# Kernel tuning notes

Hardware: AMD Instinct MI355X
Metric: run time of the kernel (lower is better)

The kernel has to match this reference:

```python
import jax, jax.numpy as jnp
import numpy as np

N = 256
IL_MMI = 0.02      # insertion loss MMI
IMB = 0.01         # imbalance MMI
IL_CR = 0.02       # insertion loss Crossing
CT = 0.01          # cross talk Crossing


def _mmi_matrix():
    # 2x2 MMI: sqrt(1-IL)*[[t, i r],[i r, t]] with t=sqrt((1+imb)/2), r=sqrt((1-imb)/2)
    a = np.sqrt(1.0 - IL_MMI)
    t = np.sqrt((1.0 + IMB) / 2.0)
    r = np.sqrt((1.0 - IMB) / 2.0)
    mmi2 = a * np.array([[t, 1j * r], [1j * r, t]], dtype=np.complex64)
    # block-diagonal over even pairs (0,1),(2,3),...
    return jnp.asarray(np.kron(np.eye(N // 2, dtype=np.complex64), mmi2))


def _crossing_matrix():
    # pairs start at odd index 1; rows 0 and N-1 pass through with amplitude sqrt(1-IL)*sqrt(1-CT)
    a = np.sqrt(1.0 - IL_CR)
    thru = a * np.sqrt(1.0 - CT)
    cr2 = a * np.array([[np.sqrt(CT), 1j * np.sqrt(1.0 - CT)],
                        [1j * np.sqrt(1.0 - CT), np.sqrt(CT)]], dtype=np.complex64)
    M = np.zeros((N, N), dtype=np.complex64)
    M[0, 0] = thru
    for i in range(1, N - 1, 2):
        M[i:i + 2, i:i + 2] = cr2
    if N % 2 == 0:
        M[-1, -1] = thru
    return jnp.asarray(M)


def setup_inputs() -> dict:
    key = jax.random.key(0)
    thetas = jax.random.uniform(key, (N // 2 + 2, N), dtype=jnp.float32) * (2.0 * np.pi)
    return {"thetas": thetas}


def reference(thetas):
    MMI = _mmi_matrix()
    CR = _crossing_matrix()
    phases = jnp.exp(1j * thetas)  # [N//2+2, N] complex64; diag phase-shift layers

    # arch = ht[0] @ I  (diagonal left-multiply == row scaling)
    arch0 = jnp.diag(phases[0])

    def body(arch, ph):
        # one mesh stage with trailing crossing (iterations i = 0 .. N//2-2)
        arch = MMI @ arch
        arch = ph[:, None] * arch      # ht[i+1] @ arch
        arch = MMI @ arch
        arch = CR @ arch
        return arch, None

    arch, _ = jax.lax.scan(body, arch0, phases[1:N // 2])

    # last loop iteration (i = N//2-1): no crossing
    arch = MMI @ arch
    arch = phases[N // 2][:, None] * arch
    arch = MMI @ arch
    # final phase layer ht[N//2+1]
    arch = phases[N // 2 + 1][:, None] * arch
    return arch
```

## Files before the change

### kernel.cpp

```cpp
#include <hip/hip_runtime.h>


__device__ __forceinline__ void sincos4(float4 th, float sn[4], float cs[4]) {
    __sincosf(th.x, &sn[0], &cs[0]);
    __sincosf(th.y, &sn[1], &cs[1]);
    __sincosf(th.z, &sn[2], &cs[2]);
    __sincosf(th.w, &sn[3], &cs[3]);
}

__global__ __launch_bounds__(64)
void neuropuls_mesh_kernel(const float* __restrict__ thetas,
                           float* __restrict__ out)
{
    constexpr int N = 256;
    const int lane = threadIdx.x;
    const int col  = blockIdx.x;

    const float AT = sqrtf(0.98f * 0.505f);
    const float AR = sqrtf(0.98f * 0.495f);
    const float BT = sqrtf(0.98f * 0.01f);
    const float BR = sqrtf(0.98f * 0.99f);

    float vr[4] = {0.f, 0.f, 0.f, 0.f};
    float vi[4] = {0.f, 0.f, 0.f, 0.f};

    {
        const float th0 = thetas[col];
        float s0, c0;
        __sincosf(th0, &s0, &c0);
        const int r0 = col - 4 * lane;
        if (0 <= r0 && r0 < 4) { vr[r0] = c0; vi[r0] = s0; }
    }

    const float* tp = thetas + N + 4 * lane;

    auto mmi_pair = [&](int x, int y) {
        float xr = vr[x], xi = vi[x], yr = vr[y], yi = vi[y];
        vr[x] = AT * xr - AR * yi;  vi[x] = AT * xi + AR * yr;
        vr[y] = AT * yr - AR * xi;  vi[y] = AT * yi + AR * xr;
    };
    auto phase4c = [&](const float sn[4], const float cs[4]) {
        #pragma unroll
        for (int j = 0; j < 4; ++j) {
            float r = vr[j], i = vi[j];
            vr[j] = cs[j] * r - sn[j] * i;
            vi[j] = cs[j] * i + sn[j] * r;
        }
    };
    auto crossing = [&]() {
        float pv3r = __shfl_up(vr[3], 1);
        float pv3i = __shfl_up(vi[3], 1);
        float nv0r = __shfl_down(vr[0], 1);
        float nv0i = __shfl_down(vi[0], 1);
        {
            float xr = vr[1], xi = vi[1], yr = vr[2], yi = vi[2];
            vr[1] = BT * xr - BR * yi;  vi[1] = BT * xi + BR * yr;
            vr[2] = BT * yr - BR * xi;  vi[2] = BT * yi + BR * xr;
        }
        {
            float yr = vr[0], yi = vi[0];
            float nr = BT * yr - BR * pv3i;
            float ni = BT * yi + BR * pv3r;
            vr[0] = (lane == 0) ? BR * yr : nr;
            vi[0] = (lane == 0) ? BR * yi : ni;
        }
        {
            float xr = vr[3], xi = vi[3];
            float nr = BT * xr - BR * nv0i;
            float ni = BT * xi + BR * nv0r;
            vr[3] = (lane == 63) ? BR * xr : nr;
            vi[3] = (lane == 63) ? BR * xi : ni;
        }
    };

    float snA[4], csA[4];
    float4 thN;
    {
        float4 t1 = *(const float4*)tp;  tp += N;
        thN = *(const float4*)tp;        tp += N;
        sincos4(t1, snA, csA);
    }

    #pragma unroll 2
    for (int s = 1; s <= 126; ++s) {
        float4 thNN = *(const float4*)tp;  tp += N;
        float snB[4], csB[4];
        sincos4(thN, snB, csB);
        mmi_pair(0, 1); mmi_pair(2, 3);
        phase4c(snA, csA);
        mmi_pair(0, 1); mmi_pair(2, 3);
        crossing();
        #pragma unroll
        for (int j = 0; j < 4; ++j) { snA[j] = snB[j]; csA[j] = csB[j]; }
        thN = thNN;
    }

    mmi_pair(0, 1); mmi_pair(2, 3);
    phase4c(snA, csA);
    mmi_pair(0, 1); mmi_pair(2, 3);
    crossing();

    {
        float sn[4], cs[4];
        sincos4(thN, sn, cs);
        float4 thF = *(const float4*)tp;
        mmi_pair(0, 1); mmi_pair(2, 3);
        phase4c(sn, cs);
        mmi_pair(0, 1); mmi_pair(2, 3);
        sincos4(thF, sn, cs);
        phase4c(sn, cs);
    }

    #pragma unroll
    for (int j = 0; j < 4; ++j) {
        const int idx = (4 * lane + j) * N + col;
        out[idx]         = vr[j];
        out[N * N + idx] = vi[j];
    }
}

extern "C" void kernel_launch(void* const* d_in, const int* in_sizes, int n_in,
                              void* d_out, int out_size, void* d_ws, size_t ws_size,
                              hipStream_t stream)
{
    const float* thetas = (const float*)d_in[0];
    float* out = (float*)d_out;
    (void)in_sizes; (void)n_in; (void)out_size; (void)d_ws; (void)ws_size;
    neuropuls_mesh_kernel<<<dim3(256), dim3(64), 0, stream>>>(thetas, out);
}
```

Baseline: 77.71 us.

## Fold MMI-phase-MMI into one precomputed 2x2 matrix and use DPP shifts

The per-stage sequence MMI, phase, MMI is folded algebraically into a single complex 2x2 matrix per pair. Its entries are computed from the next stage's sincos, off the serial dependency chain. The crossing's neighbour exchange moves from `__shfl_up`/`__shfl_down` (LDS permute) to DPP wave-shift intrinsics, and the theta prefetch goes one stage deeper. The aim is a shorter latency-bound critical path per stage, at the cost of more registers and slightly different floating-point rounding.

```diff
diff --git a/kernel.cpp b/kernel.cpp
--- a/kernel.cpp
+++ b/kernel.cpp
@@ -1,5 +1,14 @@
 #include <hip/hip_runtime.h>
 
+
+__device__ __forceinline__ float dpp_up1(float x) {
+    return __int_as_float(__builtin_amdgcn_update_dpp(
+        __float_as_int(x), __float_as_int(x), 0x138, 0xf, 0xf, false));
+}
+__device__ __forceinline__ float dpp_dn1(float x) {
+    return __int_as_float(__builtin_amdgcn_update_dpp(
+        __float_as_int(x), __float_as_int(x), 0x130, 0xf, 0xf, false));
+}
 
 __device__ __forceinline__ void sincos4(float4 th, float sn[4], float cs[4]) {
     __sincosf(th.x, &sn[0], &cs[0]);
@@ -7,6 +16,10 @@
     __sincosf(th.z, &sn[2], &cs[2]);
     __sincosf(th.w, &sn[3], &cs[3]);
 }
+
+struct Coef {
+    float Er[2], Ei[2], Fr[2], Fi[2], Gr[2], Gi[2];
+};
 
 __global__ __launch_bounds__(64)
 void neuropuls_mesh_kernel(const float* __restrict__ thetas,
@@ -16,8 +29,9 @@
     const int lane = threadIdx.x;
     const int col  = blockIdx.x;
 
-    const float AT = sqrtf(0.98f * 0.505f);
-    const float AR = sqrtf(0.98f * 0.495f);
+    const float U  = 0.98f * 0.505f;
+    const float W  = 0.98f * 0.495f;
+    const float Gc = 0.98f * sqrtf(0.505f * 0.495f);
     const float BT = sqrtf(0.98f * 0.01f);
     const float BR = sqrtf(0.98f * 0.99f);
 
@@ -34,24 +48,36 @@
 
     const float* tp = thetas + N + 4 * lane;
 
-    auto mmi_pair = [&](int x, int y) {
-        float xr = vr[x], xi = vi[x], yr = vr[y], yi = vi[y];
-        vr[x] = AT * xr - AR * yi;  vi[x] = AT * xi + AR * yr;
-        vr[y] = AT * yr - AR * xi;  vi[y] = AT * yi + AR * xr;
-    };
-    auto phase4c = [&](const float sn[4], const float cs[4]) {
+    auto prep4 = [&](float4 th, Coef& K) {
+        float s[4], c[4];
+        sincos4(th, s, c);
         #pragma unroll
-        for (int j = 0; j < 4; ++j) {
-            float r = vr[j], i = vi[j];
-            vr[j] = cs[j] * r - sn[j] * i;
-            vi[j] = cs[j] * i + sn[j] * r;
+        for (int p = 0; p < 2; ++p) {
+            const float c0 = c[2 * p], c1 = c[2 * p + 1];
+            const float s0 = s[2 * p], s1 = s[2 * p + 1];
+            K.Er[p] = U * c0 - W * c1;   K.Ei[p] = U * s0 - W * s1;
+            K.Fr[p] = U * c1 - W * c0;   K.Fi[p] = U * s1 - W * s0;
+            K.Gr[p] = -Gc * (s0 + s1);   K.Gi[p] = Gc * (c0 + c1);
         }
     };
+
+    auto mstep = [&](const Coef& K) {
+        #pragma unroll
+        for (int p = 0; p < 2; ++p) {
+            const int x = 2 * p, y = 2 * p + 1;
+            const float xr = vr[x], xi = vi[x], yr = vr[y], yi = vi[y];
+            vr[x] = K.Er[p] * xr - K.Ei[p] * xi + K.Gr[p] * yr - K.Gi[p] * yi;
+            vi[x] = K.Er[p] * xi + K.Ei[p] * xr + K.Gr[p] * yi + K.Gi[p] * yr;
+            vr[y] = K.Gr[p] * xr - K.Gi[p] * xi + K.Fr[p] * yr - K.Fi[p] * yi;
+            vi[y] = K.Gr[p] * xi + K.Gi[p] * xr + K.Fr[p] * yi + K.Fi[p] * yr;
+        }
+    };
+
     auto crossing = [&]() {
-        float pv3r = __shfl_up(vr[3], 1);
-        float pv3i = __shfl_up(vi[3], 1);
-        float nv0r = __shfl_down(vr[0], 1);
-        float nv0i = __shfl_down(vi[0], 1);
+        float pv3r = dpp_up1(vr[3]);
+        float pv3i = dpp_up1(vi[3]);
+        float nv0r = dpp_dn1(vr[0]);
+        float nv0i = dpp_dn1(vi[0]);
         {
             float xr = vr[1], xi = vi[1], yr = vr[2], yi = vi[2];
             vr[1] = BT * xr - BR * yi;  vi[1] = BT * xi + BR * yr;
@@ -73,42 +99,41 @@
         }
     };
 
-    float snA[4], csA[4];
-    float4 thN;
+    Coef KA;
+    float4 thB, thC;
     {
         float4 t1 = *(const float4*)tp;  tp += N;
-        thN = *(const float4*)tp;        tp += N;
-        sincos4(t1, snA, csA);
+        thB       = *(const float4*)tp;  tp += N;
+        thC       = *(const float4*)tp;  tp += N;
+        prep4(t1, KA);
     }
 
     #pragma unroll 2
     for (int s = 1; s <= 126; ++s) {
-        float4 thNN = *(const float4*)tp;  tp += N;
-        float snB[4], csB[4];
-        sincos4(thN, snB, csB);
-        mmi_pair(0, 1); mmi_pair(2, 3);
-        phase4c(snA, csA);
-        mmi_pair(0, 1); mmi_pair(2, 3);
+        float4 thD = *(const float4*)tp;  tp += N;
+        Coef KB;
+        prep4(thB, KB);
+        mstep(KA);
         crossing();
-        #pragma unroll
-        for (int j = 0; j < 4; ++j) { snA[j] = snB[j]; csA[j] = csB[j]; }
-        thN = thNN;
+        KA = KB;
+        thB = thC; thC = thD;
     }
 
-    mmi_pair(0, 1); mmi_pair(2, 3);
-    phase4c(snA, csA);
-    mmi_pair(0, 1); mmi_pair(2, 3);
+    mstep(KA);
     crossing();
 
     {
+        Coef KF;
+        prep4(thB, KF);
+        mstep(KF);
         float sn[4], cs[4];
-        sincos4(thN, sn, cs);
-        float4 thF = *(const float4*)tp;
-        mmi_pair(0, 1); mmi_pair(2, 3);
-        phase4c(sn, cs);
-        mmi_pair(0, 1); mmi_pair(2, 3);
-        sincos4(thF, sn, cs);
-        phase4c(sn, cs);
+        sincos4(thC, sn, cs);
+        #pragma unroll
+        for (int j = 0; j < 4; ++j) {
+            float r = vr[j], i = vi[j];
+            vr[j] = cs[j] * r - sn[j] * i;
+            vi[j] = cs[j] * i + sn[j] * r;
+        }
     }
 
     #pragma unroll
```

New measurement: 82.94 us. +6.7%, slower.

## Map one row per thread, fuse MMI-phase-MMI algebraically, use DPP and LDS staging

Applied to the files above, without the earlier changes.

Each block now uses 256 threads with one matrix row per thread instead of 64 threads holding four rows each. The MMI-phase-MMI sequence is folded into a single 2x2 complex transform whose coefficients come from the pair's sincos values, exchanged with DPP xor. All per-stage thetas are staged into LDS up front, and the crossing uses DPP shifts plus an LDS boundary exchange across waves. That exchange needs a __syncthreads every stage, which adds barrier latency to the serial 127-stage chain. The change spreads each column's work over four waves, but the 128 KB of LDS caps occupancy at one block per CU.

```diff
diff --git a/kernel.cpp b/kernel.cpp
--- a/kernel.cpp
+++ b/kernel.cpp
@@ -1,122 +1,129 @@
 #include <hip/hip_runtime.h>
 
 
-__device__ __forceinline__ void sincos4(float4 th, float sn[4], float cs[4]) {
-    __sincosf(th.x, &sn[0], &cs[0]);
-    __sincosf(th.y, &sn[1], &cs[1]);
-    __sincosf(th.z, &sn[2], &cs[2]);
-    __sincosf(th.w, &sn[3], &cs[3]);
+__device__ __forceinline__ float dpp_xor1(float x) {
+    return __int_as_float(__builtin_amdgcn_update_dpp(
+        __float_as_int(x), __float_as_int(x), 0xB1, 0xf, 0xf, false));
+}
+__device__ __forceinline__ float dpp_up1(float x) {
+    return __int_as_float(__builtin_amdgcn_update_dpp(
+        __float_as_int(x), __float_as_int(x), 0x138, 0xf, 0xf, false));
+}
+__device__ __forceinline__ float dpp_dn1(float x) {
+    return __int_as_float(__builtin_amdgcn_update_dpp(
+        __float_as_int(x), __float_as_int(x), 0x130, 0xf, 0xf, false));
 }
 
-__global__ __launch_bounds__(64)
+__global__ __launch_bounds__(256, 1)
 void neuropuls_mesh_kernel(const float* __restrict__ thetas,
                            float* __restrict__ out)
 {
     constexpr int N = 256;
-    const int lane = threadIdx.x;
+    __shared__ float thlds[128 * N];
+    __shared__ float bnd[2][4][4];
+
+    const int tid  = threadIdx.x;
+    const int lane = tid & 63;
+    const int w    = tid >> 6;
     const int col  = blockIdx.x;
 
-    const float AT = sqrtf(0.98f * 0.505f);
-    const float AR = sqrtf(0.98f * 0.495f);
+    const float U  = 0.98f * 0.505f;
+    const float W  = 0.98f * 0.495f;
+    const float Gg = 0.98f * sqrtf(0.505f * 0.495f);
     const float BT = sqrtf(0.98f * 0.01f);
     const float BR = sqrtf(0.98f * 0.99f);
 
-    float vr[4] = {0.f, 0.f, 0.f, 0.f};
-    float vi[4] = {0.f, 0.f, 0.f, 0.f};
+    {
+        const float4* s4 = (const float4*)(thetas + N);
+        float4*       d4 = (float4*)thlds;
+        #pragma unroll
+        for (int k = 0; k < 32; ++k)
+            d4[tid + k * 256] = s4[tid + k * 256];
+    }
+
+    float vr = 0.f, vi = 0.f;
+    {
+        float s0, c0;
+        __sincosf(thetas[col], &s0, &c0);
+        if (tid == col) { vr = c0; vi = s0; }
+    }
+    __syncthreads();
+
+    const bool odd  = (tid & 1) != 0;
+    const bool thru = (tid == 0) || (tid == N - 1);
+    const float* tl = thlds + tid;
+
+    auto prep = [&](float th, float& Kr, float& Ki, float& Gr, float& Gi) {
+        float s, c;
+        __sincosf(th, &s, &c);
+        const float cp = dpp_xor1(c);
+        const float sp = dpp_xor1(s);
+        Kr = U * c - W * cp;
+        Ki = U * s - W * sp;
+        Gr = -Gg * (s + sp);
+        Gi =  Gg * (c + cp);
+    };
+
+    float Kr, Ki, Gr, Gi;
+    prep(tl[0], Kr, Ki, Gr, Gi);
+    float thA = tl[256];
+
+    for (int s = 1; s <= 127; ++s) {
+        const float thB = tl[(s < 127 ? s + 1 : 127) * 256];
+        float Kr2, Ki2, Gr2, Gi2;
+        prep(thA, Kr2, Ki2, Gr2, Gi2);
+
+        {
+            const float pr = dpp_xor1(vr), pi = dpp_xor1(vi);
+            const float nr = Kr * vr - Ki * vi + Gr * pr - Gi * pi;
+            const float ni = Kr * vi + Ki * vr + Gr * pi + Gi * pr;
+            vr = nr; vi = ni;
+        }
+
+        const int p = s & 1;
+        if (lane == 0)  { bnd[p][w][0] = vr; bnd[p][w][1] = vi; }
+        if (lane == 63) { bnd[p][w][2] = vr; bnd[p][w][3] = vi; }
+        __syncthreads();
+        {
+            const float ur = dpp_up1(vr), ui = dpp_up1(vi);
+            const float dr = dpp_dn1(vr), di = dpp_dn1(vi);
+            float pr = odd ? dr : ur;
+            float pi = odd ? di : ui;
+            if (lane == 0) {
+                const int pw = (w > 0) ? w - 1 : 0;
+                pr = bnd[p][pw][2]; pi = bnd[p][pw][3];
+            }
+            if (lane == 63) {
+                const int nw = (w < 3) ? w + 1 : 3;
+                pr = bnd[p][nw][0]; pi = bnd[p][nw][1];
+            }
+            const float nr = BT * vr - BR * pi;
+            const float ni = BT * vi + BR * pr;
+            vr = thru ? BR * vr : nr;
+            vi = thru ? BR * vi : ni;
+        }
+
+        Kr = Kr2; Ki = Ki2; Gr = Gr2; Gi = Gi2;
+        thA = thB;
+    }
 
     {
-        const float th0 = thetas[col];
-        float s0, c0;
-        __sincosf(th0, &s0, &c0);
-        const int r0 = col - 4 * lane;
-        if (0 <= r0 && r0 < 4) { vr[r0] = c0; vi[r0] = s0; }
+        const float pr = dpp_xor1(vr), pi = dpp_xor1(vi);
+        const float nr = Kr * vr - Ki * vi + Gr * pr - Gi * pi;
+        const float ni = Kr * vi + Ki * vr + Gr * pi + Gi * pr;
+        vr = nr; vi = ni;
     }
 
-    const float* tp = thetas + N + 4 * lane;
-
-    auto mmi_pair = [&](int x, int y) {
-        float xr = vr[x], xi = vi[x], yr = vr[y], yi = vi[y];
-        vr[x] = AT * xr - AR * yi;  vi[x] = AT * xi + AR * yr;
-        vr[y] = AT * yr - AR * xi;  vi[y] = AT * yi + AR * xr;
-    };
-    auto phase4c = [&](const float sn[4], const float cs[4]) {
-        #pragma unroll
-        for (int j = 0; j < 4; ++j) {
-            float r = vr[j], i = vi[j];
-            vr[j] = cs[j] * r - sn[j] * i;
-            vi[j] = cs[j] * i + sn[j] * r;
-        }
-    };
-    auto crossing = [&]() {
-        float pv3r = __shfl_up(vr[3], 1);
-        float pv3i = __shfl_up(vi[3], 1);
-        float nv0r = __shfl_down(vr[0], 1);
-        float nv0i = __shfl_down(vi[0], 1);
-        {
-            float xr = vr[1], xi = vi[1], yr = vr[2], yi = vi[2];
-            vr[1] = BT * xr - BR * yi;  vi[1] = BT * xi + BR * yr;
-            vr[2] = BT * yr - BR * xi;  vi[2] = BT * yi + BR * xr;
-        }
-        {
-            float yr = vr[0], yi = vi[0];
-            float nr = BT * yr - BR * pv3i;
-            float ni = BT * yi + BR * pv3r;
-            vr[0] = (lane == 0) ? BR * yr : nr;
-            vi[0] = (lane == 0) ? BR * yi : ni;
-        }
-        {
-            float xr = vr[3], xi = vi[3];
-            float nr = BT * xr - BR * nv0i;
-            float ni = BT * xi + BR * nv0r;
-            vr[3] = (lane == 63) ? BR * xr : nr;
-            vi[3] = (lane == 63) ? BR * xi : ni;
-        }
-    };
-
-    float snA[4], csA[4];
-    float4 thN;
     {
-        float4 t1 = *(const float4*)tp;  tp += N;
-        thN = *(const float4*)tp;        tp += N;
-        sincos4(t1, snA, csA);
+        float s9, c9;
+        __sincosf(thetas[129 * N + tid], &s9, &c9);
+        const float nr = c9 * vr - s9 * vi;
+        const float ni = c9 * vi + s9 * vr;
+        vr = nr; vi = ni;
     }
 
-    #pragma unroll 2
-    for (int s = 1; s <= 126; ++s) {
-        float4 thNN = *(const float4*)tp;  tp += N;
-        float snB[4], csB[4];
-        sincos4(thN, snB, csB);
-        mmi_pair(0, 1); mmi_pair(2, 3);
-        phase4c(snA, csA);
-        mmi_pair(0, 1); mmi_pair(2, 3);
-        crossing();
-        #pragma unroll
-        for (int j = 0; j < 4; ++j) { snA[j] = snB[j]; csA[j] = csB[j]; }
-        thN = thNN;
-    }
-
-    mmi_pair(0, 1); mmi_pair(2, 3);
-    phase4c(snA, csA);
-    mmi_pair(0, 1); mmi_pair(2, 3);
-    crossing();
-
-    {
-        float sn[4], cs[4];
-        sincos4(thN, sn, cs);
-        float4 thF = *(const float4*)tp;
-        mmi_pair(0, 1); mmi_pair(2, 3);
-        phase4c(sn, cs);
-        mmi_pair(0, 1); mmi_pair(2, 3);
-        sincos4(thF, sn, cs);
-        phase4c(sn, cs);
-    }
-
-    #pragma unroll
-    for (int j = 0; j < 4; ++j) {
-        const int idx = (4 * lane + j) * N + col;
-        out[idx]         = vr[j];
-        out[N * N + idx] = vi[j];
-    }
+    out[tid * N + col]         = vr;
+    out[N * N + tid * N + col] = vi;
 }
 
 extern "C" void kernel_launch(void* const* d_in, const int* in_sizes, int n_in,
@@ -126,5 +133,5 @@
     const float* thetas = (const float*)d_in[0];
     float* out = (float*)d_out;
     (void)in_sizes; (void)n_in; (void)out_size; (void)d_ws; (void)ws_size;
-    neuropuls_mesh_kernel<<<dim3(256), dim3(64), 0, stream>>>(thetas, out);
+    neuropuls_mesh_kernel<<<dim3(256), dim3(256), 0, stream>>>(thetas, out);
 }
```

After: 90.60 us. +16.6%, slower.
